# Kernel optimization log

Hardware: AMD Instinct MI355X
Metric: run time of the kernel (lower is better)

Reference implementation:

```python
import jax, jax.numpy as jnp
import numpy as np

MARGIN = 1.0
EPS = 1e-6


def _cos(a, b):
    # Row-wise cosine similarity, matching torch.nn.CosineSimilarity semantics:
    # dot / max(||a|| * ||b||, eps)
    num = jnp.sum(a * b, axis=-1)
    den = jnp.maximum(jnp.linalg.norm(a, axis=-1) * jnp.linalg.norm(b, axis=-1), EPS)
    return num / den


def setup_inputs() -> dict:
    key = jax.random.key(0)
    k1, k2, k3 = jax.random.split(key, 3)
    B, D = 16384, 1024
    output = jax.random.normal(k1, (B, D), dtype=jnp.float32)
    target = jax.random.normal(k2, (B, D), dtype=jnp.float32)
    # offset in [0, B-1); j = (i + 1 + neg_idx) % B guarantees j != i, uniform over the rest
    neg_idx = jax.random.randint(k3, (B,), 0, B - 1, dtype=jnp.int64)
    return {"output": output, "target": target, "neg_idx": neg_idx}


def reference(output, target, neg_idx):
    B = output.shape[0]
    j = (jnp.arange(B) + 1 + neg_idx) % B  # random negative index, j != i
    t_neg = target[j]                       # gather negative label embeddings [B, D]
    hinge = jax.nn.relu(MARGIN - _cos(target, output) + _cos(t_neg, output))
    return jnp.sum(hinge) / B
```

## Files before the change

kernel.cpp:

```cpp
#include <hip/hip_runtime.h>
#include <hip/hip_bf16.h>


#define EPS 1e-6f

typedef float f4 __attribute__((ext_vector_type(4)));

#define DPP_STEP(x, ctrl, rm, bm)                                             \
    x += __int_as_float(__builtin_amdgcn_update_dpp(                          \
        0, __float_as_int(x), (ctrl), (rm), (bm), true))

__device__ __forceinline__ float dpp_wave_sum(float x) {
    DPP_STEP(x, 0x111, 0xf, 0xf);
    DPP_STEP(x, 0x112, 0xf, 0xf);
    DPP_STEP(x, 0x114, 0xf, 0xe);
    DPP_STEP(x, 0x118, 0xf, 0xc);
    DPP_STEP(x, 0x142, 0xa, 0xf);
    DPP_STEP(x, 0x143, 0xc, 0xf);
    return x;
}

__global__ __launch_bounds__(256) void hinge_cos_kernel(
    const float* __restrict__ outm,
    const float* __restrict__ tgt,
    const int*   __restrict__ negidx,
    float* __restrict__ res,
    int B, int D, float invB) {

    const int lane  = threadIdx.x & 63;
    const int wave  = threadIdx.x >> 6;
    const int wpb   = blockDim.x >> 6;
    const int gwave = blockIdx.x * wpb + wave;
    const int nwav  = gridDim.x * wpb;
    const int CH    = 4;

    float acc = 0.f;

    for (int i = gwave; i < B; i += nwav) {
        int j = i + 1 + negidx[i];
        if (j >= B) j -= B;

        const f4* o4 = (const f4*)(outm + (size_t)i * D);
        const f4* t4 = (const f4*)(tgt  + (size_t)i * D);
        const f4* n4 = (const f4*)(tgt  + (size_t)j * D);

        f4 o[CH], t[CH], n[CH];
#pragma unroll
        for (int k = 0; k < CH; ++k)
            o[k] = __builtin_nontemporal_load(&o4[lane + 64 * k]);
#pragma unroll
        for (int k = 0; k < CH; ++k) t[k] = t4[lane + 64 * k];
#pragma unroll
        for (int k = 0; k < CH; ++k) n[k] = n4[lane + 64 * k];

        float d_to = 0.f, d_no = 0.f, oo = 0.f, tt = 0.f, nn = 0.f;
#pragma unroll
        for (int k = 0; k < CH; ++k) {
            d_to += o[k].x * t[k].x + o[k].y * t[k].y + o[k].z * t[k].z + o[k].w * t[k].w;
            d_no += o[k].x * n[k].x + o[k].y * n[k].y + o[k].z * n[k].z + o[k].w * n[k].w;
            oo   += o[k].x * o[k].x + o[k].y * o[k].y + o[k].z * o[k].z + o[k].w * o[k].w;
            tt   += t[k].x * t[k].x + t[k].y * t[k].y + t[k].z * t[k].z + t[k].w * t[k].w;
            nn   += n[k].x * n[k].x + n[k].y * n[k].y + n[k].z * n[k].z + n[k].w * n[k].w;
        }

        d_to = dpp_wave_sum(d_to);
        d_no = dpp_wave_sum(d_no);
        oo   = dpp_wave_sum(oo);
        tt   = dpp_wave_sum(tt);
        nn   = dpp_wave_sum(nn);

        if (lane == 63) {
            float no   = sqrtf(oo);
            float den1 = fmaxf(sqrtf(tt) * no, EPS);
            float den2 = fmaxf(sqrtf(nn) * no, EPS);
            float hinge = 1.f - d_to / den1 + d_no / den2;
            if (hinge > 0.f) acc += hinge;
        }
    }

    __shared__ float red[4];
    if (lane == 63) red[wave] = acc;
    __syncthreads();
    if (threadIdx.x == 0) {
        float s = 0.f;
#pragma unroll
        for (int w = 0; w < 4; ++w) s += red[w];
        atomicAdd(res, s * invB);
    }
}

extern "C" void kernel_launch(void* const* d_in, const int* in_sizes, int n_in,
                              void* d_out, int out_size, void* d_ws, size_t ws_size,
                              hipStream_t stream) {
    const float* outm   = (const float*)d_in[0];
    const float* tgt    = (const float*)d_in[1];
    const int*   negidx = (const int*)d_in[2];
    float* res = (float*)d_out;

    const int B = in_sizes[2];
    const int D = in_sizes[0] / B;

    (void)hipMemsetAsync(res, 0, sizeof(float), stream);

    hinge_cos_kernel<<<2048, 256, 0, stream>>>(outm, tgt, negidx, res, B, D,
                                               1.0f / (float)B);
}
```

Before: 155.8 us.

## Software-pipeline row loads with double buffering and halve grid size

Each wave now prefetches the next row's output, target and negative-target vectors into a second register buffer while it reduces the current row. The grid is halved so each wave processes more rows, giving the prefetch loop something to overlap. This aims to hide global memory latency within a wave, at the cost of doubled register use and fewer resident waves.

```diff
diff --git a/kernel.cpp b/kernel.cpp
--- a/kernel.cpp
+++ b/kernel.cpp
@@ -20,7 +20,48 @@
     return x;
 }
 
-__global__ __launch_bounds__(256) void hinge_cos_kernel(
+struct RowBuf {
+    f4 o[4], t[4], n[4];
+};
+
+__device__ __forceinline__ void issue_loads(RowBuf& rb,
+                                            const float* __restrict__ outm,
+                                            const float* __restrict__ tgt,
+                                            int i, int j, int lane, int D) {
+    const f4* o4 = (const f4*)(outm + (size_t)i * D);
+    const f4* t4 = (const f4*)(tgt  + (size_t)i * D);
+    const f4* n4 = (const f4*)(tgt  + (size_t)j * D);
+#pragma unroll
+    for (int k = 0; k < 4; ++k)
+        rb.o[k] = __builtin_nontemporal_load(&o4[lane + 64 * k]);
+#pragma unroll
+    for (int k = 0; k < 4; ++k) rb.t[k] = t4[lane + 64 * k];
+#pragma unroll
+    for (int k = 0; k < 4; ++k) rb.n[k] = n4[lane + 64 * k];
+}
+
+__device__ __forceinline__ float consume(const RowBuf& rb) {
+    float dto = 0.f, dno = 0.f, oo = 0.f, tt = 0.f, nn = 0.f;
+#pragma unroll
+    for (int k = 0; k < 4; ++k) {
+        dto += rb.o[k].x*rb.t[k].x + rb.o[k].y*rb.t[k].y + rb.o[k].z*rb.t[k].z + rb.o[k].w*rb.t[k].w;
+        dno += rb.o[k].x*rb.n[k].x + rb.o[k].y*rb.n[k].y + rb.o[k].z*rb.n[k].z + rb.o[k].w*rb.n[k].w;
+        oo  += rb.o[k].x*rb.o[k].x + rb.o[k].y*rb.o[k].y + rb.o[k].z*rb.o[k].z + rb.o[k].w*rb.o[k].w;
+        tt  += rb.t[k].x*rb.t[k].x + rb.t[k].y*rb.t[k].y + rb.t[k].z*rb.t[k].z + rb.t[k].w*rb.t[k].w;
+        nn  += rb.n[k].x*rb.n[k].x + rb.n[k].y*rb.n[k].y + rb.n[k].z*rb.n[k].z + rb.n[k].w*rb.n[k].w;
+    }
+    dto = dpp_wave_sum(dto);
+    dno = dpp_wave_sum(dno);
+    oo  = dpp_wave_sum(oo);
+    tt  = dpp_wave_sum(tt);
+    nn  = dpp_wave_sum(nn);
+    float no = sqrtf(oo);
+    float h  = 1.f - dto / fmaxf(sqrtf(tt) * no, EPS)
+                   + dno / fmaxf(sqrtf(nn) * no, EPS);
+    return fmaxf(h, 0.f);
+}
+
+__global__ __launch_bounds__(256, 4) void hinge_cos_kernel(
     const float* __restrict__ outm,
     const float* __restrict__ tgt,
     const int*   __restrict__ negidx,
@@ -32,50 +73,28 @@
     const int wpb   = blockDim.x >> 6;
     const int gwave = blockIdx.x * wpb + wave;
     const int nwav  = gridDim.x * wpb;
-    const int CH    = 4;
 
     float acc = 0.f;
 
-    for (int i = gwave; i < B; i += nwav) {
+    RowBuf cur, nxt;
+    int i = gwave;
+    if (i < B) {
         int j = i + 1 + negidx[i];
         if (j >= B) j -= B;
-
-        const f4* o4 = (const f4*)(outm + (size_t)i * D);
-        const f4* t4 = (const f4*)(tgt  + (size_t)i * D);
-        const f4* n4 = (const f4*)(tgt  + (size_t)j * D);
-
-        f4 o[CH], t[CH], n[CH];
-#pragma unroll
-        for (int k = 0; k < CH; ++k)
-            o[k] = __builtin_nontemporal_load(&o4[lane + 64 * k]);
-#pragma unroll
-        for (int k = 0; k < CH; ++k) t[k] = t4[lane + 64 * k];
-#pragma unroll
-        for (int k = 0; k < CH; ++k) n[k] = n4[lane + 64 * k];
-
-        float d_to = 0.f, d_no = 0.f, oo = 0.f, tt = 0.f, nn = 0.f;
-#pragma unroll
-        for (int k = 0; k < CH; ++k) {
-            d_to += o[k].x * t[k].x + o[k].y * t[k].y + o[k].z * t[k].z + o[k].w * t[k].w;
-            d_no += o[k].x * n[k].x + o[k].y * n[k].y + o[k].z * n[k].z + o[k].w * n[k].w;
-            oo   += o[k].x * o[k].x + o[k].y * o[k].y + o[k].z * o[k].z + o[k].w * o[k].w;
-            tt   += t[k].x * t[k].x + t[k].y * t[k].y + t[k].z * t[k].z + t[k].w * t[k].w;
-            nn   += n[k].x * n[k].x + n[k].y * n[k].y + n[k].z * n[k].z + n[k].w * n[k].w;
+        issue_loads(cur, outm, tgt, i, j, lane, D);
+    }
+    while (i < B) {
+        const int inext = i + nwav;
+        const bool havenext = inext < B;
+        if (havenext) {
+            int jn = inext + 1 + negidx[inext];
+            if (jn >= B) jn -= B;
+            issue_loads(nxt, outm, tgt, inext, jn, lane, D);
         }
-
-        d_to = dpp_wave_sum(d_to);
-        d_no = dpp_wave_sum(d_no);
-        oo   = dpp_wave_sum(oo);
-        tt   = dpp_wave_sum(tt);
-        nn   = dpp_wave_sum(nn);
-
-        if (lane == 63) {
-            float no   = sqrtf(oo);
-            float den1 = fmaxf(sqrtf(tt) * no, EPS);
-            float den2 = fmaxf(sqrtf(nn) * no, EPS);
-            float hinge = 1.f - d_to / den1 + d_no / den2;
-            if (hinge > 0.f) acc += hinge;
-        }
+        float h = consume(cur);
+        if (lane == 63) acc += h;
+        if (havenext) cur = nxt;
+        i = inext;
     }
 
     __shared__ float red[4];
@@ -102,6 +121,6 @@
 
     (void)hipMemsetAsync(res, 0, sizeof(float), stream);
 
-    hinge_cos_kernel<<<2048, 256, 0, stream>>>(outm, tgt, negidx, res, B, D,
+    hinge_cos_kernel<<<1024, 256, 0, stream>>>(outm, tgt, negidx, res, B, D,
                                                1.0f / (float)B);
 }
```

After: 141.9 us. 1.1x faster.

## Stage row loads through LDS via global_load_lds DMA and resize grid

Applied to the files above, without the earlier changes.

Each wave now copies its output, target and negative rows into a per-wave LDS buffer with global_load_lds, waits on vmcnt, then reads them back from LDS for the dot products. The grid shrinks to 768 blocks with a launch-bounds occupancy hint of 3. The goal is to bypass register staging of loads and shape memory traffic for this bandwidth-bound reduction. The cost is extra LDS round-trips, the loss of the nontemporal hint on the output stream, and fewer waves in flight, which can hide less latency.

```diff
diff --git a/kernel.cpp b/kernel.cpp
--- a/kernel.cpp
+++ b/kernel.cpp
@@ -5,6 +5,9 @@
 #define EPS 1e-6f
 
 typedef float f4 __attribute__((ext_vector_type(4)));
+
+#define WAIT_VM0   0x0f70
+#define WAIT_LGKM0 0xc07f
 
 #define DPP_STEP(x, ctrl, rm, bm)                                             \
     x += __int_as_float(__builtin_amdgcn_update_dpp(                          \
@@ -20,19 +23,30 @@
     return x;
 }
 
-__global__ __launch_bounds__(256) void hinge_cos_kernel(
+__device__ __forceinline__ void dma16(const float* g, float* l) {
+    __builtin_amdgcn_global_load_lds(
+        (const __attribute__((address_space(1))) float*)g,
+        (__attribute__((address_space(3))) float*)l,
+        16, 0, 0);
+}
+
+__global__ __launch_bounds__(256, 3) void hinge_cos_kernel(
     const float* __restrict__ outm,
     const float* __restrict__ tgt,
     const int*   __restrict__ negidx,
     float* __restrict__ res,
     int B, int D, float invB) {
 
+    __shared__ float stage[4][3072];
+    __shared__ float red[4];
+
     const int lane  = threadIdx.x & 63;
     const int wave  = threadIdx.x >> 6;
-    const int wpb   = blockDim.x >> 6;
-    const int gwave = blockIdx.x * wpb + wave;
-    const int nwav  = gridDim.x * wpb;
-    const int CH    = 4;
+    const int gwave = blockIdx.x * 4 + wave;
+    const int nwav  = gridDim.x * 4;
+
+    float* sw = &stage[wave][0];
+    const f4* sv = (const f4*)sw;
 
     float acc = 0.f;
 
@@ -40,45 +54,49 @@
         int j = i + 1 + negidx[i];
         if (j >= B) j -= B;
 
-        const f4* o4 = (const f4*)(outm + (size_t)i * D);
-        const f4* t4 = (const f4*)(tgt  + (size_t)i * D);
-        const f4* n4 = (const f4*)(tgt  + (size_t)j * D);
+        const float* ob = outm + (size_t)i * D;
+        const float* tb = tgt  + (size_t)i * D;
+        const float* nb = tgt  + (size_t)j * D;
 
-        f4 o[CH], t[CH], n[CH];
+        __builtin_amdgcn_s_waitcnt(WAIT_LGKM0);
+
 #pragma unroll
-        for (int k = 0; k < CH; ++k)
-            o[k] = __builtin_nontemporal_load(&o4[lane + 64 * k]);
+        for (int k = 0; k < 4; ++k) dma16(ob + k * 256 + lane * 4, sw + k * 256);
 #pragma unroll
-        for (int k = 0; k < CH; ++k) t[k] = t4[lane + 64 * k];
+        for (int k = 0; k < 4; ++k) dma16(tb + k * 256 + lane * 4, sw + 1024 + k * 256);
 #pragma unroll
-        for (int k = 0; k < CH; ++k) n[k] = n4[lane + 64 * k];
+        for (int k = 0; k < 4; ++k) dma16(nb + k * 256 + lane * 4, sw + 2048 + k * 256);
 
-        float d_to = 0.f, d_no = 0.f, oo = 0.f, tt = 0.f, nn = 0.f;
+        __builtin_amdgcn_s_waitcnt(WAIT_VM0);
+        __builtin_amdgcn_sched_barrier(0);
+
+        float dto = 0.f, dno = 0.f, oo = 0.f, tt = 0.f, nn = 0.f;
 #pragma unroll
-        for (int k = 0; k < CH; ++k) {
-            d_to += o[k].x * t[k].x + o[k].y * t[k].y + o[k].z * t[k].z + o[k].w * t[k].w;
-            d_no += o[k].x * n[k].x + o[k].y * n[k].y + o[k].z * n[k].z + o[k].w * n[k].w;
-            oo   += o[k].x * o[k].x + o[k].y * o[k].y + o[k].z * o[k].z + o[k].w * o[k].w;
-            tt   += t[k].x * t[k].x + t[k].y * t[k].y + t[k].z * t[k].z + t[k].w * t[k].w;
-            nn   += n[k].x * n[k].x + n[k].y * n[k].y + n[k].z * n[k].z + n[k].w * n[k].w;
+        for (int k = 0; k < 4; ++k) {
+            f4 o = sv[      k * 64 + lane];
+            f4 t = sv[256 + k * 64 + lane];
+            f4 n = sv[512 + k * 64 + lane];
+            dto += o.x * t.x + o.y * t.y + o.z * t.z + o.w * t.w;
+            dno += o.x * n.x + o.y * n.y + o.z * n.z + o.w * n.w;
+            oo  += o.x * o.x + o.y * o.y + o.z * o.z + o.w * o.w;
+            tt  += t.x * t.x + t.y * t.y + t.z * t.z + t.w * t.w;
+            nn  += n.x * n.x + n.y * n.y + n.z * n.z + n.w * n.w;
         }
 
-        d_to = dpp_wave_sum(d_to);
-        d_no = dpp_wave_sum(d_no);
-        oo   = dpp_wave_sum(oo);
-        tt   = dpp_wave_sum(tt);
-        nn   = dpp_wave_sum(nn);
+        dto = dpp_wave_sum(dto);
+        dno = dpp_wave_sum(dno);
+        oo  = dpp_wave_sum(oo);
+        tt  = dpp_wave_sum(tt);
+        nn  = dpp_wave_sum(nn);
 
         if (lane == 63) {
-            float no   = sqrtf(oo);
-            float den1 = fmaxf(sqrtf(tt) * no, EPS);
-            float den2 = fmaxf(sqrtf(nn) * no, EPS);
-            float hinge = 1.f - d_to / den1 + d_no / den2;
-            if (hinge > 0.f) acc += hinge;
+            float no = sqrtf(oo);
+            float h  = 1.f - dto / fmaxf(sqrtf(tt) * no, EPS)
+                           + dno / fmaxf(sqrtf(nn) * no, EPS);
+            acc += fmaxf(h, 0.f);
         }
     }
 
-    __shared__ float red[4];
     if (lane == 63) red[wave] = acc;
     __syncthreads();
     if (threadIdx.x == 0) {
@@ -102,6 +120,6 @@
 
     (void)hipMemsetAsync(res, 0, sizeof(float), stream);
 
-    hinge_cos_kernel<<<2048, 256, 0, stream>>>(outm, tgt, negidx, res, B, D,
-                                               1.0f / (float)B);
+    hinge_cos_kernel<<<768, 256, 0, stream>>>(outm, tgt, negidx, res, B, D,
+                                              1.0f / (float)B);
 }
```

Measured after the change: 151.3 us. -2.9%, faster.
